# Performance work log

Measured on AMD Instinct MI355X. Metric: run time of the kernel, lower is better.

The kernel has to match this reference:

```python
import jax, jax.numpy as jnp
import numpy as np

D_MODEL = 1024
N_HEADS = 16
HEAD_DIM = D_MODEL // N_HEADS  # 64
BASE = 10000.0
MAX_X, MAX_Y, MAX_Z = 32, 32, 8
NEG_INF = -1e9  # stand-in for float('-inf') in masked_fill; identical after softmax


def _split_dims(head_dim):
    n_pairs = head_dim // 2
    px = n_pairs // 3
    py = n_pairs // 3
    pz = n_pairs - px - py
    return px * 2, py * 2, pz * 2


def _cos_sin_table(dim, max_pos):
    # matches RotaryEmbedding3D._register_cache
    inv_freq = 1.0 / (BASE ** (np.arange(0, dim, 2, dtype=np.float32) / dim))
    t = np.arange(max_pos, dtype=np.float32)[:, None] * inv_freq  # [max_pos, dim/2]
    cos = np.repeat(np.cos(t), 2, axis=-1)  # repeat_interleave(2)
    sin = np.repeat(np.sin(t), 2, axis=-1)
    return jnp.asarray(cos), jnp.asarray(sin)


def _rotate_half(x):
    x1 = x[..., ::2]
    x2 = x[..., 1::2]
    return jnp.stack((-x2, x1), axis=-1).reshape(x.shape)


def setup_inputs() -> dict:
    key = jax.random.key(0)
    k1, k2, k3, k4, k5, k6 = jax.random.split(key, 6)
    B, S = 2, 2048
    hidden_states = jax.random.normal(k1, (B, S, D_MODEL), dtype=jnp.float32)
    w_qkv = jax.random.normal(k2, (D_MODEL, 3 * D_MODEL), dtype=jnp.float32) * 0.02
    w_out = jax.random.normal(k3, (D_MODEL, D_MODEL), dtype=jnp.float32) * 0.02
    px = jax.random.randint(k4, (B, S, 1), 0, MAX_X)
    py = jax.random.randint(k5, (B, S, 1), 0, MAX_Y)
    pz = jax.random.randint(k6, (B, S, 1), 0, MAX_Z)
    pos_xyz = jnp.concatenate([px, py, pz], axis=-1).astype(jnp.int64)
    causal_mask = jnp.triu(jnp.ones((S, S), dtype=bool), k=1)[None, None]  # [1,1,S,S]
    return {"hidden_states": hidden_states, "w_qkv": w_qkv, "w_out": w_out,
            "pos_xyz": pos_xyz, "causal_mask": causal_mask}


def reference(hidden_states, w_qkv, w_out, pos_xyz, causal_mask):
    B, S, D = hidden_states.shape
    H, Hd = N_HEADS, HEAD_DIM
    # fused QKV projection
    qkv = hidden_states @ w_qkv  # [B,S,3D]
    qkv = qkv.reshape(B, S, 3, H, Hd).transpose(2, 0, 3, 1, 4)  # [3,B,H,S,Hd]
    q, k, v = qkv[0], qkv[1], qkv[2]
    # 3D RoPE tables and lookups
    dx, dy, dz = _split_dims(Hd)
    cx, sx = _cos_sin_table(dx, MAX_X)
    cy, sy = _cos_sin_table(dy, MAX_Y)
    cz, sz = _cos_sin_table(dz, MAX_Z)
    ix = jnp.clip(pos_xyz[..., 0], 0, MAX_X - 1)
    iy = jnp.clip(pos_xyz[..., 1], 0, MAX_Y - 1)
    iz = jnp.clip(pos_xyz[..., 2], 0, MAX_Z - 1)
    cos = jnp.concatenate([cx[ix], cy[iy], cz[iz]], axis=-1)[:, None]  # [B,1,S,Hd]
    sin = jnp.concatenate([sx[ix], sy[iy], sz[iz]], axis=-1)[:, None]
    q = q * cos + _rotate_half(q) * sin
    k = k * cos + _rotate_half(k) * sin
    # SDPA with causal bias
    scale = Hd ** -0.5
    scores = jnp.einsum('bhqd,bhkd->bhqk', q, k) * scale
    scores = jnp.where(causal_mask, jnp.asarray(NEG_INF, scores.dtype), scores)
    probs = jax.nn.softmax(scores, axis=-1)
    attn = jnp.einsum('bhqk,bhkd->bhqd', probs, v)
    attn = attn.transpose(0, 2, 1, 3).reshape(B, S, D)
    return attn @ w_out
```

## Files before the change

kernel.cpp:

```cpp
#include <hip/hip_runtime.h>
#include <hip/hip_bf16.h>
#include <math.h>

typedef __bf16 bf16;
typedef __bf16 bf16x8 __attribute__((ext_vector_type(8)));
typedef float f32x4 __attribute__((ext_vector_type(4)));

#define SEQ 2048
#define NHEADS 16
#define HDIM 64
#define DM 1024
#define QKVW 3072

__device__ __forceinline__ void gload_lds16(const void* g, void* l) {
  __builtin_amdgcn_global_load_lds(
      (const __attribute__((address_space(1))) unsigned int*)g,
      (__attribute__((address_space(3))) unsigned int*)l, 16, 0, 0);
}

template <int CTRL>
__device__ __forceinline__ float dppmovf(float x) {
  return __builtin_bit_cast(
      float, __builtin_amdgcn_mov_dpp(__builtin_bit_cast(int, x), CTRL, 0xf,
                                      0xf, true));
}
__device__ __forceinline__ float rowsum16(float x) {
  x += dppmovf<0xB1>(x);
  x += dppmovf<0x4E>(x);
  x += dppmovf<0x124>(x);
  x += dppmovf<0x128>(x);
  return x;
}

__global__ __launch_bounds__(256) void prep(
    const float* __restrict__ hidden, const float* __restrict__ w_qkv,
    const float* __restrict__ w_out, const int* __restrict__ pos,
    bf16* __restrict__ hid_bf, bf16* __restrict__ wqkvT,
    bf16* __restrict__ woutT, float2* __restrict__ tbl) {
  __shared__ float tile[64][65];
  int idx = blockIdx.x, tid = threadIdx.x;
  if (idx < 2048) {
    int i = (idx * 256 + tid) * 8;
    float4 a = *(const float4*)(hidden + i);
    float4 b = *(const float4*)(hidden + i + 4);
    bf16x8 o;
    o[0] = (bf16)a.x; o[1] = (bf16)a.y; o[2] = (bf16)a.z; o[3] = (bf16)a.w;
    o[4] = (bf16)b.x; o[5] = (bf16)b.y; o[6] = (bf16)b.z; o[7] = (bf16)b.w;
    *(bf16x8*)(hid_bf + i) = o;
  } else if (idx < 3072) {
    const float* in; bf16* out; int R, C, t;
    if (idx < 2816) { t = idx - 2048; in = w_qkv; out = wqkvT; R = 1024; C = 3072; }
    else            { t = idx - 2816; in = w_out; out = woutT; R = 1024; C = 1024; }
    int nbx = C >> 6;
    int c0 = (t % nbx) * 64, r0 = (t / nbx) * 64;
    int col = tid & 63, rb = (tid >> 6) * 16;
#pragma unroll
    for (int i = 0; i < 16; ++i)
      tile[rb + i][col] = in[(size_t)(r0 + rb + i) * C + c0 + col];
    __syncthreads();
#pragma unroll
    for (int i = 0; i < 16; ++i)
      out[(size_t)(c0 + rb + i) * R + r0 + col] = (bf16)tile[col][rb + i];
  } else {
    const float LN1E4 = 9.210340371976184f;
    int gi = (idx - 3072) * 256 + tid;
    int m = gi >> 5, pr = gi & 31;
    int axis, d, iloc;
    if (pr < 10)      { axis = 0; d = 20; iloc = pr; }
    else if (pr < 20) { axis = 1; d = 20; iloc = pr - 10; }
    else              { axis = 2; d = 24; iloc = pr - 20; }
    int p = pos[m * 3 + axis];
    int pmax = (axis == 2) ? 7 : 31;
    p = p < 0 ? 0 : (p > pmax ? pmax : p);
    float invf = __expf(-((float)(2 * iloc) / (float)d) * LN1E4);
    float sn, cs;
    __sincosf((float)p * invf, &sn, &cs);
    tbl[gi] = make_float2(cs, sn);
  }
}

__global__ __launch_bounds__(256) void post_qkv(
    bf16* __restrict__ qkv, const float2* __restrict__ tbl,
    bf16* __restrict__ vT) {
  __shared__ bf16 btile[64][65];
  int idx = blockIdx.x, tid = threadIdx.x;
  if (idx < 2048) {
    int gi = idx * 256 + tid;
    int m = gi >> 7, seg = gi & 127;
    bf16* p = qkv + (size_t)m * QKVW + seg * 16;
    bf16x8 a = *(const bf16x8*)p;
    bf16x8 b2 = *(const bf16x8*)(p + 8);
    const float2* t = tbl + m * 32 + (((seg * 16) & 63) >> 1);
#pragma unroll
    for (int j = 0; j < 4; ++j) {
      float2 cs = t[j];
      float e = (float)a[2 * j], o = (float)a[2 * j + 1];
      a[2 * j]     = (bf16)(e * cs.x - o * cs.y);
      a[2 * j + 1] = (bf16)(o * cs.x + e * cs.y);
    }
#pragma unroll
    for (int j = 0; j < 4; ++j) {
      float2 cs = t[4 + j];
      float e = (float)b2[2 * j], o = (float)b2[2 * j + 1];
      b2[2 * j]     = (bf16)(e * cs.x - o * cs.y);
      b2[2 * j + 1] = (bf16)(o * cs.x + e * cs.y);
    }
    *(bf16x8*)p = a;
    *(bf16x8*)(p + 8) = b2;
  } else {
    int t = idx - 2048;
    int s0 = (t & 31) * 64, bh = t >> 5;
    int b = bh >> 4, h = bh & 15;
    const bf16* src = qkv + (size_t)(b * SEQ + s0) * QKVW + 2 * DM + h * 64;
    int col = tid & 63, rb = (tid >> 6) * 16;
#pragma unroll
    for (int i = 0; i < 16; ++i)
      btile[rb + i][col] = src[(size_t)(rb + i) * QKVW + col];
    __syncthreads();
    bf16* dst = vT + (size_t)bh * HDIM * SEQ + s0;
#pragma unroll
    for (int i = 0; i < 16; ++i)
      dst[(size_t)(rb + i) * SEQ + col] = btile[col][rb + i];
  }
}

__global__ __launch_bounds__(256) void gemm_bt(
    const bf16* __restrict__ A, const bf16* __restrict__ Bt,
    bf16* __restrict__ C, int M, int N, int K) {
  __shared__ __align__(16) bf16 a_lds[128 * 32];
  __shared__ __align__(16) bf16 b_lds[128 * 32];
  int tid = threadIdx.x;
  int wave = tid >> 6, lane = tid & 63;
  int quad = lane >> 4, l15 = lane & 15;
  int wm = wave >> 1, wn = wave & 1;

  int flat = blockIdx.y * gridDim.x + blockIdx.x;
  int mband = gridDim.y >> 3;
  int xcd = flat & 7, sidx = flat >> 3;
  int m0 = (xcd * mband + (sidx % mband)) * 128;
  int n0 = (sidx / mband) * 128;

  f32x4 acc[4][4] = {};

  for (int kt = 0; kt < K; kt += 32) {
    __syncthreads();
#pragma unroll
    for (int call = 0; call < 2; ++call) {
      int chunk = call * 256 + tid;
      int row = chunk >> 2, cc = (chunk & 3) * 8;
      gload_lds16(A + (size_t)(m0 + row) * K + kt + cc,
                  (char*)a_lds + call * 4096 + wave * 1024);
      gload_lds16(Bt + (size_t)(n0 + row) * K + kt + cc,
                  (char*)b_lds + call * 4096 + wave * 1024);
    }
    __syncthreads();
    bf16x8 af[4], bfr[4];
#pragma unroll
    for (int i = 0; i < 4; ++i) {
      af[i]  = *(const bf16x8*)(a_lds + (wm * 64 + i * 16 + l15) * 32 + quad * 8);
      bfr[i] = *(const bf16x8*)(b_lds + (wn * 64 + i * 16 + l15) * 32 + quad * 8);
    }
#pragma unroll
    for (int mi = 0; mi < 4; ++mi)
#pragma unroll
      for (int ni = 0; ni < 4; ++ni)
        acc[mi][ni] = __builtin_amdgcn_mfma_f32_16x16x32_bf16(
            af[mi], bfr[ni], acc[mi][ni], 0, 0, 0);
  }

#pragma unroll
  for (int mi = 0; mi < 4; ++mi) {
    int mb = m0 + wm * 64 + mi * 16 + quad * 4;
#pragma unroll
    for (int ni = 0; ni < 4; ++ni) {
      int n = n0 + wn * 64 + ni * 16 + l15;
#pragma unroll
      for (int r = 0; r < 4; ++r)
        C[(size_t)(mb + r) * N + n] = (bf16)acc[mi][ni][r];
    }
  }
}

__global__ __launch_bounds__(256) void gemm_bt64(
    const bf16* __restrict__ A, const bf16* __restrict__ Bt,
    float* __restrict__ C, int M, int N, int K) {
  __shared__ __align__(16) bf16 a_lds[64 * 32];
  __shared__ __align__(16) bf16 b_lds[128 * 32];
  int tid = threadIdx.x;
  int wave = tid >> 6, lane = tid & 63;
  int quad = lane >> 4, l15 = lane & 15;
  int wm = wave >> 1, wn = wave & 1;

  int flat = blockIdx.y * gridDim.x + blockIdx.x;
  int mband = gridDim.y >> 3;
  int xcd = flat & 7, sidx = flat >> 3;
  int m0 = (xcd * mband + (sidx % mband)) * 64;
  int n0 = (sidx / mband) * 128;

  f32x4 acc[2][4] = {};

  for (int kt = 0; kt < K; kt += 32) {
    __syncthreads();
    {
      int row = tid >> 2, cc = (tid & 3) * 8;
      gload_lds16(A + (size_t)(m0 + row) * K + kt + cc,
                  (char*)a_lds + wave * 1024);
    }
#pragma unroll
    for (int call = 0; call < 2; ++call) {
      int chunk = call * 256 + tid;
      int row = chunk >> 2, cc = (chunk & 3) * 8;
      gload_lds16(Bt + (size_t)(n0 + row) * K + kt + cc,
                  (char*)b_lds + call * 4096 + wave * 1024);
    }
    __syncthreads();
    bf16x8 af[2], bfr[4];
#pragma unroll
    for (int i = 0; i < 2; ++i)
      af[i] = *(const bf16x8*)(a_lds + (wm * 32 + i * 16 + l15) * 32 + quad * 8);
#pragma unroll
    for (int i = 0; i < 4; ++i)
      bfr[i] = *(const bf16x8*)(b_lds + (wn * 64 + i * 16 + l15) * 32 + quad * 8);
#pragma unroll
    for (int mi = 0; mi < 2; ++mi)
#pragma unroll
      for (int ni = 0; ni < 4; ++ni)
        acc[mi][ni] = __builtin_amdgcn_mfma_f32_16x16x32_bf16(
            af[mi], bfr[ni], acc[mi][ni], 0, 0, 0);
  }

#pragma unroll
  for (int mi = 0; mi < 2; ++mi) {
    int mb = m0 + wm * 32 + mi * 16 + quad * 4;
#pragma unroll
    for (int ni = 0; ni < 4; ++ni) {
      int n = n0 + wn * 64 + ni * 16 + l15;
#pragma unroll
      for (int r = 0; r < 4; ++r)
        C[(size_t)(mb + r) * N + n] = acc[mi][ni][r];
    }
  }
}

__global__ __launch_bounds__(256, 4) void attn_fwd(
    const bf16* __restrict__ QKV, const bf16* __restrict__ VT,
    bf16* __restrict__ O) {
  __shared__ __align__(16) bf16 k_lds[2][64 * 72];
  __shared__ __align__(16) bf16 p_lds[4][16 * 72];
  const float C2 = 0.18033688011112042f;
  const float C3 = -5.770780163555854f;
  int tid = threadIdx.x;
  int wave = tid >> 6, lane = tid & 63;
  int quad = lane >> 4, l15 = lane & 15;
  int idx = blockIdx.x;
  int bh = idx & 31;
  int g = idx >> 5;
  int qt = (g < 16) ? (31 - g) : (g - 16);
  int q0 = qt * 64;
  int b = bh >> 4, h = bh & 15;
  const bf16* Qb = QKV + (size_t)b * SEQ * QKVW + h * 64;
  const bf16* Kb = Qb + DM;
  const bf16* VTb = VT + (size_t)bh * HDIM * SEQ;
  bf16* pw = p_lds[wave];

  const bf16* qr = Qb + (size_t)(q0 + wave * 16 + l15) * QKVW;
  bf16x8 qf0 = *(const bf16x8*)(qr + quad * 8);
  bf16x8 qf1 = *(const bf16x8*)(qr + 32 + quad * 8);

  int r0c = tid >> 3, off0 = (tid & 7) * 8;

  const bf16* vrow[4];
#pragma unroll
  for (int nt = 0; nt < 4; ++nt)
    vrow[nt] = VTb + (size_t)(nt * 16 + l15) * SEQ + quad * 8;

  int niter = qt + 1;
  f32x4 o_acc[4] = {};
  float lsum[4] = {};
  int qrow[4];
#pragma unroll
  for (int r = 0; r < 4; ++r) qrow[r] = q0 + wave * 16 + quad * 4 + r;

  bf16x8 kpre0 = *(const bf16x8*)(Kb + (size_t)r0c * QKVW + off0);
  bf16x8 kpre1 = *(const bf16x8*)(Kb + (size_t)(r0c + 32) * QKVW + off0);

  for (int tkv = 0; tkv < niter; ++tkv) {
    int kv0 = tkv * 64;
    bf16* kb = k_lds[tkv & 1];
    *(bf16x8*)(kb + r0c * 72 + off0) = kpre0;
    *(bf16x8*)(kb + (r0c + 32) * 72 + off0) = kpre1;
    __syncthreads();
    bf16x8 vf0[4], vf1[4];
#pragma unroll
    for (int nt = 0; nt < 4; ++nt) {
      vf0[nt] = *(const bf16x8*)(vrow[nt] + kv0);
      vf1[nt] = *(const bf16x8*)(vrow[nt] + kv0 + 32);
    }
    if (tkv + 1 < niter) {
      int kn = kv0 + 64;
      kpre0 = *(const bf16x8*)(Kb + (size_t)(kn + r0c) * QKVW + off0);
      kpre1 = *(const bf16x8*)(Kb + (size_t)(kn + r0c + 32) * QKVW + off0);
    }
    f32x4 s_acc[4];
#pragma unroll
    for (int nt = 0; nt < 4; ++nt) {
      const bf16* kr = kb + (nt * 16 + l15) * 72;
      bf16x8 kf0 = *(const bf16x8*)(kr + quad * 8);
      bf16x8 kf1 = *(const bf16x8*)(kr + 32 + quad * 8);
      f32x4 z = {};
      z = __builtin_amdgcn_mfma_f32_16x16x32_bf16(qf0, kf0, z, 0, 0, 0);
      z = __builtin_amdgcn_mfma_f32_16x16x32_bf16(qf1, kf1, z, 0, 0, 0);
      s_acc[nt] = z;
    }
    bool diag = (tkv == qt);
#pragma unroll
    for (int r = 0; r < 4; ++r) {
#pragma unroll
      for (int nt = 0; nt < 4; ++nt) {
        float p = __builtin_amdgcn_exp2f(s_acc[nt][r] * C2 + C3);
        if (diag && (kv0 + nt * 16 + l15 > qrow[r])) p = 0.f;
        lsum[r] += p;
        pw[(quad * 4 + r) * 72 + nt * 16 + l15] = (bf16)p;
      }
    }
    __asm__ volatile("s_waitcnt lgkmcnt(0)" ::: "memory");
    bf16x8 pf0 = *(const bf16x8*)(pw + l15 * 72 + quad * 8);
    bf16x8 pf1 = *(const bf16x8*)(pw + l15 * 72 + 32 + quad * 8);
#pragma unroll
    for (int nt = 0; nt < 4; ++nt) {
      o_acc[nt] = __builtin_amdgcn_mfma_f32_16x16x32_bf16(pf0, vf0[nt], o_acc[nt], 0, 0, 0);
      o_acc[nt] = __builtin_amdgcn_mfma_f32_16x16x32_bf16(pf1, vf1[nt], o_acc[nt], 0, 0, 0);
    }
  }
#pragma unroll
  for (int r = 0; r < 4; ++r) {
    float inv = 1.f / rowsum16(lsum[r]);
    int sq = qrow[r];
#pragma unroll
    for (int nt = 0; nt < 4; ++nt)
      O[((size_t)(b * SEQ + sq)) * DM + h * HDIM + nt * 16 + l15] =
          (bf16)(o_acc[nt][r] * inv);
  }
}

extern "C" void kernel_launch(void* const* d_in, const int* in_sizes, int n_in,
                              void* d_out, int out_size, void* d_ws,
                              size_t ws_size, hipStream_t stream) {
  const float* hidden = (const float*)d_in[0];
  const float* w_qkv  = (const float*)d_in[1];
  const float* w_out  = (const float*)d_in[2];
  const int*   pos    = (const int*)d_in[3];
  float* out = (float*)d_out;

  char* ws = (char*)d_ws;
  bf16* wqkvT  = (bf16*)ws;  ws += (size_t)3072 * 1024 * 2;
  bf16* woutT  = (bf16*)ws;  ws += (size_t)1024 * 1024 * 2;
  bf16* hid_bf = (bf16*)ws;  ws += (size_t)4096 * 1024 * 2;
  bf16* qkv_ws = (bf16*)ws;  ws += (size_t)4096 * 3072 * 2;
  bf16* vT_ws  = (bf16*)ws;  ws += (size_t)32 * SEQ * HDIM * 2;
  float2* ropetbl = (float2*)ws;
  bf16* attn_ws = hid_bf;

  prep<<<dim3(3584), 256, 0, stream>>>(hidden, w_qkv, w_out, pos,
                                       hid_bf, wqkvT, woutT, ropetbl);
  gemm_bt<<<dim3(24, 32), 256, 0, stream>>>(
      hid_bf, wqkvT, qkv_ws, 4096, 3072, 1024);
  post_qkv<<<dim3(3072), 256, 0, stream>>>(qkv_ws, ropetbl, vT_ws);
  attn_fwd<<<dim3(1024), 256, 0, stream>>>(qkv_ws, vT_ws, attn_ws);
  gemm_bt64<<<dim3(8, 64), 256, 0, stream>>>(
      attn_ws, woutT, out, 4096, 1024, 1024);
}
```

Before: 228.5 us.

## Rewrite attention with 32x32 MFMA, transposed scores, and LDS-staged V

The attention kernel now uses 128-thread blocks of two waves, each owning 32 query rows, and 32x32x16 bf16 MFMAs. Scores are computed transposed (K as A, Q as B), so the exponentiated P tile stays in registers and feeds the PV MFMA directly. This drops the per-wave P round trip through LDS. V tiles are double-buffered in LDS next to K, and the row sums are computed by an MFMA against a ones vector instead of DPP reductions, with s_setprio hints around the MFMA sections. In exchange there is more register pressure, fewer threads per block, and extra MFMA work for the row sums.

```diff
diff --git a/kernel.cpp b/kernel.cpp
--- a/kernel.cpp
+++ b/kernel.cpp
@@ -3,8 +3,11 @@
 #include <math.h>
 
 typedef __bf16 bf16;
+typedef __bf16 bf16x4 __attribute__((ext_vector_type(4)));
 typedef __bf16 bf16x8 __attribute__((ext_vector_type(8)));
 typedef float f32x4 __attribute__((ext_vector_type(4)));
+typedef float f32x16 __attribute__((ext_vector_type(16)));
+typedef int i32x4 __attribute__((ext_vector_type(4)));
 
 #define SEQ 2048
 #define NHEADS 16
@@ -18,18 +21,10 @@
       (__attribute__((address_space(3))) unsigned int*)l, 16, 0, 0);
 }
 
-template <int CTRL>
-__device__ __forceinline__ float dppmovf(float x) {
-  return __builtin_bit_cast(
-      float, __builtin_amdgcn_mov_dpp(__builtin_bit_cast(int, x), CTRL, 0xf,
-                                      0xf, true));
-}
-__device__ __forceinline__ float rowsum16(float x) {
-  x += dppmovf<0xB1>(x);
-  x += dppmovf<0x4E>(x);
-  x += dppmovf<0x124>(x);
-  x += dppmovf<0x128>(x);
-  return x;
+__device__ __forceinline__ int pk2(float a, float b) {
+  union { __bf16 h; unsigned short u; } ua, ub;
+  ua.h = (__bf16)a; ub.h = (__bf16)b;
+  return (int)ua.u | ((int)ub.u << 16);
 }
 
 __global__ __launch_bounds__(256) void prep(
@@ -242,16 +237,16 @@
   }
 }
 
-__global__ __launch_bounds__(256, 4) void attn_fwd(
+__global__ __launch_bounds__(128) void attn_fwd(
     const bf16* __restrict__ QKV, const bf16* __restrict__ VT,
     bf16* __restrict__ O) {
   __shared__ __align__(16) bf16 k_lds[2][64 * 72];
-  __shared__ __align__(16) bf16 p_lds[4][16 * 72];
+  __shared__ __align__(16) bf16 v_lds[2][64 * 72];
   const float C2 = 0.18033688011112042f;
   const float C3 = -5.770780163555854f;
   int tid = threadIdx.x;
-  int wave = tid >> 6, lane = tid & 63;
-  int quad = lane >> 4, l15 = lane & 15;
+  int w = tid >> 6, lane = tid & 63;
+  int l31 = lane & 31, hi = lane >> 5;
   int idx = blockIdx.x;
   int bh = idx & 31;
   int g = idx >> 5;
@@ -261,85 +256,104 @@
   const bf16* Qb = QKV + (size_t)b * SEQ * QKVW + h * 64;
   const bf16* Kb = Qb + DM;
   const bf16* VTb = VT + (size_t)bh * HDIM * SEQ;
-  bf16* pw = p_lds[wave];
-
-  const bf16* qr = Qb + (size_t)(q0 + wave * 16 + l15) * QKVW;
-  bf16x8 qf0 = *(const bf16x8*)(qr + quad * 8);
-  bf16x8 qf1 = *(const bf16x8*)(qr + 32 + quad * 8);
-
-  int r0c = tid >> 3, off0 = (tid & 7) * 8;
-
-  const bf16* vrow[4];
-#pragma unroll
-  for (int nt = 0; nt < 4; ++nt)
-    vrow[nt] = VTb + (size_t)(nt * 16 + l15) * SEQ + quad * 8;
+
+  int qg = q0 + w * 32 + l31;
+  const bf16* qr = Qb + (size_t)qg * QKVW;
+  bf16x8 qf[4];
+#pragma unroll
+  for (int j = 0; j < 4; ++j)
+    qf[j] = *(const bf16x8*)(qr + j * 16 + hi * 8);
+
+  i32x4 onesi = {0x3F803F80, 0x3F803F80, 0x3F803F80, 0x3F803F80};
+  bf16x8 onesf = __builtin_bit_cast(bf16x8, onesi);
+
+  int r16 = tid >> 3, off0 = (tid & 7) * 8;
 
   int niter = qt + 1;
-  f32x4 o_acc[4] = {};
-  float lsum[4] = {};
-  int qrow[4];
-#pragma unroll
-  for (int r = 0; r < 4; ++r) qrow[r] = q0 + wave * 16 + quad * 4 + r;
-
-  bf16x8 kpre0 = *(const bf16x8*)(Kb + (size_t)r0c * QKVW + off0);
-  bf16x8 kpre1 = *(const bf16x8*)(Kb + (size_t)(r0c + 32) * QKVW + off0);
+  f32x16 oT[2] = {};
+  f32x16 accl = {};
+
+  bf16x8 kpre[4], vpre[4];
+#pragma unroll
+  for (int p = 0; p < 4; ++p) {
+    kpre[p] = *(const bf16x8*)(Kb + (size_t)(r16 + p * 16) * QKVW + off0);
+    vpre[p] = *(const bf16x8*)(VTb + (size_t)(r16 + p * 16) * SEQ + off0);
+  }
 
   for (int tkv = 0; tkv < niter; ++tkv) {
     int kv0 = tkv * 64;
     bf16* kb = k_lds[tkv & 1];
-    *(bf16x8*)(kb + r0c * 72 + off0) = kpre0;
-    *(bf16x8*)(kb + (r0c + 32) * 72 + off0) = kpre1;
-    __syncthreads();
-    bf16x8 vf0[4], vf1[4];
-#pragma unroll
-    for (int nt = 0; nt < 4; ++nt) {
-      vf0[nt] = *(const bf16x8*)(vrow[nt] + kv0);
-      vf1[nt] = *(const bf16x8*)(vrow[nt] + kv0 + 32);
-    }
+    bf16* vb = v_lds[tkv & 1];
+#pragma unroll
+    for (int p = 0; p < 4; ++p) {
+      *(bf16x8*)(kb + (r16 + p * 16) * 72 + off0) = kpre[p];
+      *(bf16x8*)(vb + (r16 + p * 16) * 72 + off0) = vpre[p];
+    }
+    __syncthreads();
     if (tkv + 1 < niter) {
       int kn = kv0 + 64;
-      kpre0 = *(const bf16x8*)(Kb + (size_t)(kn + r0c) * QKVW + off0);
-      kpre1 = *(const bf16x8*)(Kb + (size_t)(kn + r0c + 32) * QKVW + off0);
-    }
-    f32x4 s_acc[4];
-#pragma unroll
-    for (int nt = 0; nt < 4; ++nt) {
-      const bf16* kr = kb + (nt * 16 + l15) * 72;
-      bf16x8 kf0 = *(const bf16x8*)(kr + quad * 8);
-      bf16x8 kf1 = *(const bf16x8*)(kr + 32 + quad * 8);
-      f32x4 z = {};
-      z = __builtin_amdgcn_mfma_f32_16x16x32_bf16(qf0, kf0, z, 0, 0, 0);
-      z = __builtin_amdgcn_mfma_f32_16x16x32_bf16(qf1, kf1, z, 0, 0, 0);
-      s_acc[nt] = z;
-    }
+#pragma unroll
+      for (int p = 0; p < 4; ++p) {
+        kpre[p] = *(const bf16x8*)(Kb + (size_t)(kn + r16 + p * 16) * QKVW + off0);
+        vpre[p] = *(const bf16x8*)(VTb + (size_t)(r16 + p * 16) * SEQ + kn + off0);
+      }
+    }
+    f32x16 sT[2] = {};
+    __builtin_amdgcn_s_setprio(1);
+#pragma unroll
+    for (int c = 0; c < 2; ++c)
+#pragma unroll
+      for (int j = 0; j < 4; ++j) {
+        bf16x8 kf = *(const bf16x8*)(kb + (c * 32 + l31) * 72 + j * 16 + hi * 8);
+        sT[c] = __builtin_amdgcn_mfma_f32_32x32x16_bf16(kf, qf[j], sT[c], 0, 0, 0);
+      }
+    __builtin_amdgcn_s_setprio(0);
     bool diag = (tkv == qt);
 #pragma unroll
-    for (int r = 0; r < 4; ++r) {
-#pragma unroll
-      for (int nt = 0; nt < 4; ++nt) {
-        float p = __builtin_amdgcn_exp2f(s_acc[nt][r] * C2 + C3);
-        if (diag && (kv0 + nt * 16 + l15 > qrow[r])) p = 0.f;
-        lsum[r] += p;
-        pw[(quad * 4 + r) * 72 + nt * 16 + l15] = (bf16)p;
+    for (int c = 0; c < 2; ++c) {
+      float pv[16];
+#pragma unroll
+      for (int r = 0; r < 16; ++r)
+        pv[r] = __builtin_amdgcn_exp2f(sT[c][r] * C2 + C3);
+      if (diag) {
+#pragma unroll
+        for (int r = 0; r < 16; ++r) {
+          int kvg = kv0 + c * 32 + (r & 3) + 8 * (r >> 2) + 4 * hi;
+          if (kvg > qg) pv[r] = 0.f;
+        }
       }
-    }
-    __asm__ volatile("s_waitcnt lgkmcnt(0)" ::: "memory");
-    bf16x8 pf0 = *(const bf16x8*)(pw + l15 * 72 + quad * 8);
-    bf16x8 pf1 = *(const bf16x8*)(pw + l15 * 72 + 32 + quad * 8);
-#pragma unroll
-    for (int nt = 0; nt < 4; ++nt) {
-      o_acc[nt] = __builtin_amdgcn_mfma_f32_16x16x32_bf16(pf0, vf0[nt], o_acc[nt], 0, 0, 0);
-      o_acc[nt] = __builtin_amdgcn_mfma_f32_16x16x32_bf16(pf1, vf1[nt], o_acc[nt], 0, 0, 0);
-    }
-  }
-#pragma unroll
-  for (int r = 0; r < 4; ++r) {
-    float inv = 1.f / rowsum16(lsum[r]);
-    int sq = qrow[r];
-#pragma unroll
-    for (int nt = 0; nt < 4; ++nt)
-      O[((size_t)(b * SEQ + sq)) * DM + h * HDIM + nt * 16 + l15] =
-          (bf16)(o_acc[nt][r] * inv);
+      i32x4 w0 = {pk2(pv[0], pv[1]), pk2(pv[2], pv[3]),
+                  pk2(pv[4], pv[5]), pk2(pv[6], pv[7])};
+      i32x4 w1 = {pk2(pv[8], pv[9]),  pk2(pv[10], pv[11]),
+                  pk2(pv[12], pv[13]), pk2(pv[14], pv[15])};
+      bf16x8 pa0 = __builtin_bit_cast(bf16x8, w0);
+      bf16x8 pa1 = __builtin_bit_cast(bf16x8, w1);
+      __builtin_amdgcn_s_setprio(1);
+      accl = __builtin_amdgcn_mfma_f32_32x32x16_bf16(pa0, onesf, accl, 0, 0, 0);
+      accl = __builtin_amdgcn_mfma_f32_32x32x16_bf16(pa1, onesf, accl, 0, 0, 0);
+#pragma unroll
+      for (int m = 0; m < 2; ++m) {
+        const bf16* vd = vb + (m * 32 + l31) * 72 + c * 32 + 4 * hi;
+        bf16x4 a0 = *(const bf16x4*)(vd);
+        bf16x4 a1 = *(const bf16x4*)(vd + 8);
+        bf16x8 vf0 = __builtin_shufflevector(a0, a1, 0, 1, 2, 3, 4, 5, 6, 7);
+        oT[m] = __builtin_amdgcn_mfma_f32_32x32x16_bf16(pa0, vf0, oT[m], 0, 0, 0);
+        bf16x4 b0 = *(const bf16x4*)(vd + 16);
+        bf16x4 b1 = *(const bf16x4*)(vd + 24);
+        bf16x8 vf1 = __builtin_shufflevector(b0, b1, 0, 1, 2, 3, 4, 5, 6, 7);
+        oT[m] = __builtin_amdgcn_mfma_f32_32x32x16_bf16(pa1, vf1, oT[m], 0, 0, 0);
+      }
+      __builtin_amdgcn_s_setprio(0);
+    }
+  }
+#pragma unroll
+  for (int r = 0; r < 16; ++r) {
+    float inv = 1.f / accl[r];
+    int sq = q0 + w * 32 + (r & 3) + 8 * (r >> 2) + 4 * hi;
+#pragma unroll
+    for (int m = 0; m < 2; ++m)
+      O[(size_t)(b * SEQ + sq) * DM + h * HDIM + m * 32 + l31] =
+          (bf16)(oT[m][r] * inv);
   }
 }
 
@@ -366,7 +380,7 @@
   gemm_bt<<<dim3(24, 32), 256, 0, stream>>>(
       hid_bf, wqkvT, qkv_ws, 4096, 3072, 1024);
   post_qkv<<<dim3(3072), 256, 0, stream>>>(qkv_ws, ropetbl, vT_ws);
-  attn_fwd<<<dim3(1024), 256, 0, stream>>>(qkv_ws, vT_ws, attn_ws);
+  attn_fwd<<<dim3(1024), 128, 0, stream>>>(qkv_ws, vT_ws, attn_ws);
   gemm_bt64<<<dim3(8, 64), 256, 0, stream>>>(
       attn_ws, woutT, out, 4096, 1024, 1024);
 }
```

New measurement: 205.3 us. -10.1%, faster.
